# Kernel optimization log

Hardware: AMD Instinct MI355X
Metric: run time of the kernel (lower is better)

The kernel has to match this reference:

```python
import jax, jax.numpy as jnp
import numpy as np

N_NODES = 100000
HIDDEN = 64
N_LAYERS = 4
N_EDGES = 800000
EPS = 1e-5  # equinox RMSNorm default


def rmsnorm(x, w):
    # per-node RMSNorm over last dim, learned scale, no bias
    inv = jax.lax.rsqrt(jnp.mean(x * x, axis=-1, keepdims=True) + EPS)
    return x * inv * w


def setup_inputs() -> dict:
    key = jax.random.key(0)
    ks = jax.random.split(key, 5)
    x = jax.random.normal(ks[0], (N_NODES, HIDDEN), dtype=jnp.float32)
    # eqx Linear weight (out,in), init ~ U(-1/sqrt(in), 1/sqrt(in)); randn*scale is fine for a baseline
    scale = 1.0 / np.sqrt(HIDDEN)
    conv_w = jax.random.normal(ks[1], (N_LAYERS, HIDDEN, HIDDEN), dtype=jnp.float32) * scale
    hid_w = jax.random.normal(ks[2], (N_LAYERS, HIDDEN, HIDDEN), dtype=jnp.float32) * scale
    conv_norm_w = jnp.ones((N_LAYERS, HIDDEN), dtype=jnp.float32)
    hid_norm_w = jnp.ones((N_LAYERS, HIDDEN), dtype=jnp.float32)
    row = jax.random.randint(ks[3], (N_EDGES,), 0, N_NODES, dtype=jnp.int32)
    col = jax.random.randint(ks[4], (N_EDGES,), 0, N_NODES, dtype=jnp.int32)
    return {"x": x, "conv_w": conv_w, "conv_norm_w": conv_norm_w,
            "hid_w": hid_w, "hid_norm_w": hid_norm_w, "row": row, "col": col}


def reference(x, conv_w, conv_norm_w, hid_w, hid_norm_w, row, col):
    n_nodes = x.shape[0]

    def step(h, params):
        cw, cnw, hw, hnw = params
        # GConvLayer: linear (no bias) -> relu -> sparse adjacency aggregation -> residual RMSNorm
        m = jax.nn.relu(h @ cw.T)                                  # [n_nodes, d]
        agg = jax.ops.segment_sum(m[col], row, num_segments=n_nodes)  # a @ m (unweighted COO)
        h = rmsnorm(h + agg, cnw)
        # HiddenLayer: linear -> relu -> residual RMSNorm
        y = jax.nn.relu(h @ hw.T)
        h = rmsnorm(h + y, hnw)
        return h, None

    x, _ = jax.lax.scan(step, x, (conv_w, conv_norm_w, hid_w, hid_norm_w))
    return x
```

## Files before the change

kernel.cpp:

```cpp
#include <hip/hip_runtime.h>
#include <hip/hip_bf16.h>

#define HIDDEN 64
#define EPS 1e-5f
#define NPB 64
#define FNPB 32
#define WST 72

typedef __attribute__((ext_vector_type(8))) short bf16x8;
typedef __attribute__((ext_vector_type(4))) float f32x4;

__device__ __forceinline__ unsigned short f2b(float x) {
    __hip_bfloat16 b = __float2bfloat16(x);
    return *(unsigned short*)&b;
}
__device__ __forceinline__ float b2f(unsigned short u) {
    unsigned int ui = (unsigned int)u << 16;
    return *(float*)&ui;
}
__device__ __forceinline__ float b2f_lo(unsigned int u) { unsigned int ui = u << 16; return *(float*)&ui; }
__device__ __forceinline__ float b2f_hi(unsigned int u) { unsigned int ui = u & 0xffff0000u; return *(float*)&ui; }
__device__ __forceinline__ unsigned int pk2(float a, float b) {
    return (unsigned int)f2b(a) | ((unsigned int)f2b(b) << 16);
}


__global__ __launch_bounds__(256) void hist_rank_kernel(const int* __restrict__ row,
                                                        int* __restrict__ cnt,
                                                        int* __restrict__ erank, int e) {
    int stride = gridDim.x * blockDim.x;
    for (int i = blockIdx.x * blockDim.x + threadIdx.x; i < e; i += stride) {
        int r = row[i];
        erank[i] = atomicAdd(&cnt[r], 1);
    }
}

__global__ __launch_bounds__(256) void block_sum_kernel(const int* __restrict__ cnt,
                                                        int* __restrict__ bsum, int n) {
    __shared__ int wsum[4];
    int tid = threadIdx.x;
    int i = blockIdx.x * 256 + tid;
    int v = (i < n) ? cnt[i] : 0;
#pragma unroll
    for (int off = 32; off > 0; off >>= 1) v += __shfl_xor(v, off, 64);
    if ((tid & 63) == 0) wsum[tid >> 6] = v;
    __syncthreads();
    if (tid == 0) bsum[blockIdx.x] = wsum[0] + wsum[1] + wsum[2] + wsum[3];
}

__global__ __launch_bounds__(256) void scan_final_kernel(const int* __restrict__ cnt,
                                                         const int* __restrict__ bsum,
                                                         int* __restrict__ row_ptr,
                                                         int n, int nb) {
    __shared__ int wred[4];
    __shared__ int wsum[4];
    __shared__ int wexcl[4];
    __shared__ int s_prev;
    __shared__ int s_tot;
    int b = blockIdx.x;
    int tid = threadIdx.x;
    int lane = tid & 63;
    int w = tid >> 6;
    int acc = 0;
    for (int j = tid; j < b; j += 256) acc += bsum[j];
#pragma unroll
    for (int off = 32; off > 0; off >>= 1) acc += __shfl_xor(acc, off, 64);
    if (lane == 0) wred[w] = acc;
    int i = b * 256 + tid;
    int v = (i < n) ? cnt[i] : 0;
    int sc = v;
#pragma unroll
    for (int off = 1; off < 64; off <<= 1) {
        int t = __shfl_up(sc, off, 64);
        if (lane >= off) sc += t;
    }
    if (lane == 63) wsum[w] = sc;
    __syncthreads();
    if (tid == 0) {
        s_prev = wred[0] + wred[1] + wred[2] + wred[3];
        int a = 0;
#pragma unroll
        for (int j = 0; j < 4; j++) { wexcl[j] = a; a += wsum[j]; }
        s_tot = a;
    }
    __syncthreads();
    if (i < n) row_ptr[i] = s_prev + wexcl[w] + (sc - v);
    if (b == nb - 1 && tid == 0) row_ptr[n] = s_prev + s_tot;
}

__global__ __launch_bounds__(256) void fill_kernel(const int* __restrict__ row,
                                                   const int* __restrict__ col,
                                                   const int* __restrict__ row_ptr,
                                                   const int* __restrict__ erank,
                                                   int* __restrict__ ecol, int e, int n) {
    int cls = blockIdx.x & 7;
    int sub = blockIdx.x >> 3;
    int nsub = gridDim.x >> 3;
    int lo = (int)(((long long)n * cls) >> 3);
    int hi = (int)(((long long)n * (cls + 1)) >> 3);
    for (int i = sub * 256 + threadIdx.x; i < e; i += nsub * 256) {
        int r = row[i];
        if (r >= lo && r < hi) {
            int pos = row_ptr[r] + erank[i];
            ecol[pos] = col[i];
        }
    }
}

__global__ __launch_bounds__(256) void wconv_kernel(const float* __restrict__ cw,
                                                    const float* __restrict__ hw,
                                                    unsigned short* __restrict__ wbt,
                                                    unsigned short* __restrict__ mA,
                                                    unsigned short* __restrict__ mB,
                                                    int L, int n) {
    int idx = blockIdx.x * blockDim.x + threadIdx.x;
    int total = 2 * L * 4096;
    if (idx < total) {
        int mat = idx >> 12;
        int rem = idx & 4095;
        const float* src = (mat < L) ? (cw + (size_t)mat * 4096) : (hw + (size_t)(mat - L) * 4096);
        wbt[idx] = f2b(src[rem]);
    } else if (idx < total + HIDDEN) {
        int k = idx - total;
        mA[(size_t)n * HIDDEN + k] = 0;
        mB[(size_t)n * HIDDEN + k] = 0;
    }
}


__device__ __forceinline__ void mfma_tile(const unsigned short* s_a,
                                          const unsigned short* s_b,
                                          int l16, int quad, int wbase, f32x4 acc[4]) {
    const unsigned short* ap = &s_a[(size_t)(wbase + l16) * WST + quad * 8];
    const unsigned short* bp = &s_b[(size_t)l16 * WST + quad * 8];
#pragma unroll
    for (int kt = 0; kt < 2; kt++) {
        bf16x8 a = *(const bf16x8*)(ap + kt * 32);
#pragma unroll
        for (int nt = 0; nt < 4; nt++) {
            bf16x8 b = *(const bf16x8*)(bp + (size_t)nt * 16 * WST + kt * 32);
            acc[nt] = __builtin_amdgcn_mfma_f32_16x16x32_bf16(a, b, acc[nt], 0, 0, 0);
        }
    }
}

__device__ __forceinline__ void load_wfrag(const unsigned short* __restrict__ w,
                                           int l16, int quad, bf16x8 wf[8]) {
    const unsigned short* wp = w + (size_t)l16 * 64 + quad * 8;
#pragma unroll
    for (int nt = 0; nt < 4; nt++) {
#pragma unroll
        for (int kt = 0; kt < 2; kt++)
            wf[nt * 2 + kt] = *(const bf16x8*)(wp + (size_t)nt * 16 * 64 + kt * 32);
    }
}

__device__ __forceinline__ void stage_wb(const unsigned short* __restrict__ wsrc,
                                         unsigned short* s_wb, int tid) {
    for (int i = tid; i < 512; i += 256) {
        int r = i >> 3, seg = i & 7;
        *(uint4*)(&s_wb[r * WST + seg * 8]) = ((const uint4*)(wsrc + r * 64))[seg];
    }
}

__device__ __forceinline__ void acc8(float* p, uint4 u) {
    p[0] += b2f_lo(u.x);
    p[1] += b2f_hi(u.x);
    p[2] += b2f_lo(u.y);
    p[3] += b2f_hi(u.y);
    p[4] += b2f_lo(u.z);
    p[5] += b2f_hi(u.z);
    p[6] += b2f_lo(u.w);
    p[7] += b2f_hi(u.w);
}


__global__ __launch_bounds__(256) void mm_relu_kernel(const float* __restrict__ h,
                                                      const unsigned short* __restrict__ wb,
                                                      __hip_bfloat16* __restrict__ m, int n) {
    __shared__ unsigned short s_hb[NPB * WST];
    __shared__ unsigned short s_wb[64 * WST];
    int tid = threadIdx.x;
    int base = blockIdx.x * NPB;
    stage_wb(wb, s_wb, tid);
    for (int i = tid; i < 512; i += 256) {
        int r = i >> 3, seg = i & 7;
        if (base + r < n) {
            const float4* hp = (const float4*)(h + (size_t)(base + r) * HIDDEN + seg * 8);
            float4 ha = hp[0], hb = hp[1];
            uint4 p;
            p.x = pk2(ha.x, ha.y);
            p.y = pk2(ha.z, ha.w);
            p.z = pk2(hb.x, hb.y);
            p.w = pk2(hb.z, hb.w);
            *(uint4*)(&s_hb[r * WST + seg * 8]) = p;
        } else {
            *(uint4*)(&s_hb[r * WST + seg * 8]) = make_uint4(0u, 0u, 0u, 0u);
        }
    }
    __syncthreads();
    int lane = tid & 63, wave = tid >> 6;
    int quad = lane >> 4, l16 = lane & 15;
    int wbase = wave * 16;
    f32x4 acc[4];
    acc[0] = (f32x4){0.f,0.f,0.f,0.f}; acc[1] = (f32x4){0.f,0.f,0.f,0.f};
    acc[2] = (f32x4){0.f,0.f,0.f,0.f}; acc[3] = (f32x4){0.f,0.f,0.f,0.f};
    mfma_tile(s_hb, s_wb, l16, quad, wbase, acc);
    unsigned short* mo = (unsigned short*)m;
#pragma unroll
    for (int r = 0; r < 4; r++) {
        int node = base + wbase + quad * 4 + r;
        if (node < n) {
#pragma unroll
            for (int nt = 0; nt < 4; nt++)
                mo[(size_t)node * HIDDEN + nt * 16 + l16] = f2b(fmaxf(acc[nt][r], 0.f));
        }
    }
}


__global__ __launch_bounds__(128, 6) void fused_layer_kernel(
        const float* hf, const __hip_bfloat16* hb_in,
        const __hip_bfloat16* __restrict__ m_in,
        const unsigned short* __restrict__ hwb,
        const unsigned short* cwb_next,
        const int* __restrict__ row_ptr, const int* __restrict__ ecol,
        const float* __restrict__ cnw, const float* __restrict__ hnw,
        float* out_f32, __hip_bfloat16* hb_new, __hip_bfloat16* m_out, int n) {
    __shared__ unsigned short s_hb[FNPB * WST];
    int tid = threadIdx.x;
    int base = blockIdx.x * FNPB;
    int lane = tid & 63, wave = tid >> 6;

    int g = lane >> 2;
    int sl = lane & 3;
    int gb = lane & ~3;
    int nl = wave * 16 + g;
    int node = base + nl;

    const unsigned short* mi = (const unsigned short*)m_in;

    uint4 q0 = make_uint4(0u, 0u, 0u, 0u);
    uint4 q1 = make_uint4(0u, 0u, 0u, 0u);
    if (node < n) {
        float p[16];
        if (hf) {
            const float4* hp = (const float4*)(hf + (size_t)node * HIDDEN + 16 * sl);
            float4 v0 = hp[0], v1 = hp[1], v2 = hp[2], v3 = hp[3];
            p[0]=v0.x;  p[1]=v0.y;  p[2]=v0.z;  p[3]=v0.w;
            p[4]=v1.x;  p[5]=v1.y;  p[6]=v1.z;  p[7]=v1.w;
            p[8]=v2.x;  p[9]=v2.y;  p[10]=v2.z; p[11]=v2.w;
            p[12]=v3.x; p[13]=v3.y; p[14]=v3.z; p[15]=v3.w;
        } else {
            const uint4* hp = (const uint4*)((const unsigned short*)hb_in + (size_t)node * HIDDEN + 16 * sl);
            uint4 u0 = hp[0], u1 = hp[1];
            p[0]=b2f_lo(u0.x);  p[1]=b2f_hi(u0.x);
            p[2]=b2f_lo(u0.y);  p[3]=b2f_hi(u0.y);
            p[4]=b2f_lo(u0.z);  p[5]=b2f_hi(u0.z);
            p[6]=b2f_lo(u0.w);  p[7]=b2f_hi(u0.w);
            p[8]=b2f_lo(u1.x);  p[9]=b2f_hi(u1.x);
            p[10]=b2f_lo(u1.y); p[11]=b2f_hi(u1.y);
            p[12]=b2f_lo(u1.z); p[13]=b2f_hi(u1.z);
            p[14]=b2f_lo(u1.w); p[15]=b2f_hi(u1.w);
        }
        int beg = row_ptr[node];
        int end = row_ptr[node + 1];
        int myc = 0;
        if (beg < end) {
            int idx = beg + sl;
            myc = ecol[idx < end ? idx : end - 1];
        }
        for (int b0 = beg; b0 < end; b0 += 4) {
            int nxt = b0 + 4;
            int nmyc = 0;
            if (nxt < end) {
                int idx = nxt + sl;
                nmyc = ecol[idx < end ? idx : end - 1];
            }
            int cnt = end - b0;
            int cj[4];
#pragma unroll
            for (int j = 0; j < 4; j++) {
                int c = __shfl(myc, gb + j, 64);
                cj[j] = (j < cnt) ? c : n;
            }
            uint4 ua[4], ub[4];
#pragma unroll
            for (int j = 0; j < 4; j++) {
                const uint4* mp = (const uint4*)(mi + (size_t)cj[j] * HIDDEN + 16 * sl);
                ua[j] = mp[0];
                ub[j] = mp[1];
            }
#pragma unroll
            for (int j = 0; j < 4; j++) {
                acc8(p, ua[j]);
                acc8(p + 8, ub[j]);
            }
            myc = nmyc;
        }
        float ss = 0.f;
#pragma unroll
        for (int k = 0; k < 16; k++) ss += p[k] * p[k];
        ss += __shfl_xor(ss, 1, 64);
        ss += __shfl_xor(ss, 2, 64);
        float inv = rsqrtf(ss * (1.0f / 64.0f) + EPS);
        const float4* cp = (const float4*)(cnw + 16 * sl);
        float4 c0 = cp[0], c1 = cp[1], c2 = cp[2], c3 = cp[3];
        q0.x = pk2(p[0]*inv*c0.x,  p[1]*inv*c0.y);
        q0.y = pk2(p[2]*inv*c0.z,  p[3]*inv*c0.w);
        q0.z = pk2(p[4]*inv*c1.x,  p[5]*inv*c1.y);
        q0.w = pk2(p[6]*inv*c1.z,  p[7]*inv*c1.w);
        q1.x = pk2(p[8]*inv*c2.x,  p[9]*inv*c2.y);
        q1.y = pk2(p[10]*inv*c2.z, p[11]*inv*c2.w);
        q1.z = pk2(p[12]*inv*c3.x, p[13]*inv*c3.y);
        q1.w = pk2(p[14]*inv*c3.z, p[15]*inv*c3.w);
    }
    *(uint4*)(&s_hb[(size_t)nl * WST + 16 * sl]) = q0;
    *(uint4*)(&s_hb[(size_t)nl * WST + 16 * sl + 8]) = q1;

    int quad = lane >> 4, l16 = lane & 15;
    int wbase = wave * 16;
    bf16x8 wfh[8];
    load_wfrag(hwb, l16, quad, wfh);
    f32x4 acc[4];
    acc[0] = (f32x4){0.f,0.f,0.f,0.f}; acc[1] = (f32x4){0.f,0.f,0.f,0.f};
    acc[2] = (f32x4){0.f,0.f,0.f,0.f}; acc[3] = (f32x4){0.f,0.f,0.f,0.f};
    {
        const unsigned short* ap = &s_hb[(size_t)(wbase + l16) * WST + quad * 8];
#pragma unroll
        for (int kt = 0; kt < 2; kt++) {
            bf16x8 a = *(const bf16x8*)(ap + kt * 32);
#pragma unroll
            for (int nt = 0; nt < 4; nt++)
                acc[nt] = __builtin_amdgcn_mfma_f32_16x16x32_bf16(a, wfh[nt * 2 + kt], acc[nt], 0, 0, 0);
        }
    }

    float hv[4][4];
    float ssq[4] = {0.f, 0.f, 0.f, 0.f};
#pragma unroll
    for (int r = 0; r < 4; r++) {
        int nr = wbase + quad * 4 + r;
#pragma unroll
        for (int nt = 0; nt < 4; nt++) {
            float hres = b2f(s_hb[(size_t)nr * WST + nt * 16 + l16]);
            float v = hres + fmaxf(acc[nt][r], 0.f);
            hv[r][nt] = v;
            ssq[r] += v * v;
        }
    }
#pragma unroll
    for (int mk = 1; mk <= 8; mk <<= 1) {
#pragma unroll
        for (int r = 0; r < 4; r++) ssq[r] += __shfl_xor(ssq[r], mk, 64);
    }
    bf16x8 wfc[8];
    if (m_out) load_wfrag(cwb_next, l16, quad, wfc);
    float nwv[4];
#pragma unroll
    for (int nt = 0; nt < 4; nt++) nwv[nt] = hnw[nt * 16 + l16];
#pragma unroll
    for (int r = 0; r < 4; r++) {
        float inv = rsqrtf(ssq[r] * (1.0f / 64.0f) + EPS);
#pragma unroll
        for (int nt = 0; nt < 4; nt++) hv[r][nt] *= inv * nwv[nt];
    }
    if (out_f32) {
#pragma unroll
        for (int r = 0; r < 4; r++) {
            int nd = base + wbase + quad * 4 + r;
            if (nd < n) {
#pragma unroll
                for (int nt = 0; nt < 4; nt++)
                    out_f32[(size_t)nd * HIDDEN + nt * 16 + l16] = hv[r][nt];
            }
        }
    }
    if (hb_new) {
        unsigned short* ho = (unsigned short*)hb_new;
#pragma unroll
        for (int r = 0; r < 4; r++) {
            int nd = base + wbase + quad * 4 + r;
            if (nd < n) {
#pragma unroll
                for (int nt = 0; nt < 4; nt++)
                    ho[(size_t)nd * HIDDEN + nt * 16 + l16] = f2b(hv[r][nt]);
            }
        }
    }

    if (!m_out) return;

#pragma unroll
    for (int r = 0; r < 4; r++) {
        int nr = wbase + quad * 4 + r;
#pragma unroll
        for (int nt = 0; nt < 4; nt++)
            s_hb[(size_t)nr * WST + nt * 16 + l16] = f2b(hv[r][nt]);
    }

    f32x4 acc2[4];
    acc2[0] = (f32x4){0.f,0.f,0.f,0.f}; acc2[1] = (f32x4){0.f,0.f,0.f,0.f};
    acc2[2] = (f32x4){0.f,0.f,0.f,0.f}; acc2[3] = (f32x4){0.f,0.f,0.f,0.f};
    {
        const unsigned short* ap = &s_hb[(size_t)(wbase + l16) * WST + quad * 8];
#pragma unroll
        for (int kt = 0; kt < 2; kt++) {
            bf16x8 a = *(const bf16x8*)(ap + kt * 32);
#pragma unroll
            for (int nt = 0; nt < 4; nt++)
                acc2[nt] = __builtin_amdgcn_mfma_f32_16x16x32_bf16(a, wfc[nt * 2 + kt], acc2[nt], 0, 0, 0);
        }
    }
    unsigned short* mo = (unsigned short*)m_out;
#pragma unroll
    for (int r = 0; r < 4; r++) {
        int nd = base + wbase + quad * 4 + r;
        if (nd < n) {
#pragma unroll
            for (int nt = 0; nt < 4; nt++)
                mo[(size_t)nd * HIDDEN + nt * 16 + l16] = f2b(fmaxf(acc2[nt][r], 0.f));
        }
    }
}


static inline size_t align_up(size_t x, size_t a) { return (x + a - 1) & ~(a - 1); }

extern "C" void kernel_launch(void* const* d_in, const int* in_sizes, int n_in,
                              void* d_out, int out_size, void* d_ws, size_t ws_size,
                              hipStream_t stream) {
    const float* x       = (const float*)d_in[0];
    const float* conv_w  = (const float*)d_in[1];
    const float* conv_nw = (const float*)d_in[2];
    const float* hid_w   = (const float*)d_in[3];
    const float* hid_nw  = (const float*)d_in[4];
    const int*   row     = (const int*)d_in[5];
    const int*   col     = (const int*)d_in[6];
    float* out = (float*)d_out;

    const int n = in_sizes[0] / HIDDEN;
    const int e = in_sizes[5];
    const int L = in_sizes[1] / 4096;

    size_t off = 0;
    char* ws = (char*)d_ws;
    __hip_bfloat16* mA = (__hip_bfloat16*)(ws + off);  off = align_up(off + (size_t)(n + 1) * HIDDEN * 2, 16);
    __hip_bfloat16* mB = (__hip_bfloat16*)(ws + off);  off = align_up(off + (size_t)(n + 1) * HIDDEN * 2, 16);
    __hip_bfloat16* hb1 = (__hip_bfloat16*)(ws + off); off = align_up(off + (size_t)n * HIDDEN * 2, 16);
    __hip_bfloat16* hb2 = (__hip_bfloat16*)(ws + off); off = align_up(off + (size_t)n * HIDDEN * 2, 16);
    unsigned short* wbt = (unsigned short*)(ws + off); off = align_up(off + (size_t)2 * L * 4096 * 2, 16);
    int* row_ptr = (int*)(ws + off);           off = align_up(off + (size_t)(n + 1) * 4, 16);
    int* cnt = (int*)(ws + off);               off = align_up(off + (size_t)n * 4, 16);
    int* bsum = (int*)(ws + off);              off = align_up(off + (size_t)1024 * 4, 16);
    int* erank = (int*)(ws + off);             off = align_up(off + (size_t)e * 4, 16);
    int* ecol = (int*)(ws + off);              off = align_up(off + (size_t)e * 4, 16);

    const int nb = (n + 255) / 256;

    hipMemsetAsync(cnt, 0, (size_t)n * 4, stream);
    hist_rank_kernel<<<1024, 256, 0, stream>>>(row, cnt, erank, e);
    block_sum_kernel<<<nb, 256, 0, stream>>>(cnt, bsum, n);
    scan_final_kernel<<<nb, 256, 0, stream>>>(cnt, bsum, row_ptr, n, nb);
    fill_kernel<<<1024, 256, 0, stream>>>(row, col, row_ptr, erank, ecol, e, n);

    wconv_kernel<<<(2 * L * 4096 + HIDDEN + 255) / 256, 256, 0, stream>>>(
        conv_w, hid_w, wbt, (unsigned short*)mA, (unsigned short*)mB, L, n);

    mm_relu_kernel<<<(n + NPB - 1) / NPB, 256, 0, stream>>>(x, wbt, mA, n);

    const int fblocks = (n + FNPB - 1) / FNPB;
    const __hip_bfloat16* mi = mA;
    __hip_bfloat16* mo = mB;
    __hip_bfloat16* hin = nullptr;
    __hip_bfloat16* hout = hb1;
    for (int l = 0; l < L; l++) {
        bool last = (l == L - 1);
        fused_layer_kernel<<<fblocks, 128, 0, stream>>>(
            (l == 0) ? x : nullptr, hin, mi,
            wbt + (size_t)(L + l) * 4096,
            last ? nullptr : (wbt + (size_t)(l + 1) * 4096),
            row_ptr, ecol,
            conv_nw + (size_t)l * HIDDEN, hid_nw + (size_t)l * HIDDEN,
            last ? out : nullptr,
            last ? nullptr : hout,
            last ? nullptr : mo, n);
        __hip_bfloat16* tmp = (__hip_bfloat16*)mi; mi = mo; mo = tmp;
        hin = hout;
        hout = (hout == hb1) ? hb2 : hb1;
    }
}
```

Baseline: 296.6 us.

## Merge CSR build into cooperative kernel and use 8 lanes per node in gather

Folds the memset, histogram, two scan passes, fill and weight conversion into one cooperative kernel separated by grid syncs, which cuts launch count. The fused layer kernel now uses 256 threads with 8 lanes per node, each handling 8 features and 8 edges per step. This gives more memory-level parallelism in the gather but half-fills each MFMA tile with padded zero rows. The fill pass also drops the row-range partitioning, so its writes become scattered.

New measurement: 798.3 us. 169% more time.

```diff
diff --git a/kernel.cpp b/kernel.cpp
--- a/kernel.cpp
+++ b/kernel.cpp
@@ -1,5 +1,8 @@
 #include <hip/hip_runtime.h>
 #include <hip/hip_bf16.h>
+#include <hip/hip_cooperative_groups.h>
+
+namespace cg = cooperative_groups;
 
 #define HIDDEN 64
 #define EPS 1e-5f
@@ -25,105 +28,88 @@
 }
 
 
-__global__ __launch_bounds__(256) void hist_rank_kernel(const int* __restrict__ row,
-                                                        int* __restrict__ cnt,
-                                                        int* __restrict__ erank, int e) {
-    int stride = gridDim.x * blockDim.x;
-    for (int i = blockIdx.x * blockDim.x + threadIdx.x; i < e; i += stride) {
-        int r = row[i];
-        erank[i] = atomicAdd(&cnt[r], 1);
-    }
-}
-
-__global__ __launch_bounds__(256) void block_sum_kernel(const int* __restrict__ cnt,
-                                                        int* __restrict__ bsum, int n) {
+__global__ __launch_bounds__(256) void csr_coop_kernel(
+        const int* __restrict__ row, const int* __restrict__ col,
+        const float* __restrict__ cw, const float* __restrict__ hw,
+        int* cnt, int* erank, int* bsum, int* row_ptr, int* ecol,
+        unsigned short* wbt, unsigned short* mA, unsigned short* mB,
+        int n, int e, int L, int nb) {
+    cg::grid_group grid = cg::this_grid();
     __shared__ int wsum[4];
-    int tid = threadIdx.x;
-    int i = blockIdx.x * 256 + tid;
-    int v = (i < n) ? cnt[i] : 0;
-#pragma unroll
-    for (int off = 32; off > 0; off >>= 1) v += __shfl_xor(v, off, 64);
-    if ((tid & 63) == 0) wsum[tid >> 6] = v;
-    __syncthreads();
-    if (tid == 0) bsum[blockIdx.x] = wsum[0] + wsum[1] + wsum[2] + wsum[3];
-}
-
-__global__ __launch_bounds__(256) void scan_final_kernel(const int* __restrict__ cnt,
-                                                         const int* __restrict__ bsum,
-                                                         int* __restrict__ row_ptr,
-                                                         int n, int nb) {
     __shared__ int wred[4];
-    __shared__ int wsum[4];
     __shared__ int wexcl[4];
     __shared__ int s_prev;
     __shared__ int s_tot;
-    int b = blockIdx.x;
     int tid = threadIdx.x;
-    int lane = tid & 63;
-    int w = tid >> 6;
-    int acc = 0;
-    for (int j = tid; j < b; j += 256) acc += bsum[j];
-#pragma unroll
-    for (int off = 32; off > 0; off >>= 1) acc += __shfl_xor(acc, off, 64);
-    if (lane == 0) wred[w] = acc;
-    int i = b * 256 + tid;
-    int v = (i < n) ? cnt[i] : 0;
-    int sc = v;
-#pragma unroll
-    for (int off = 1; off < 64; off <<= 1) {
-        int t = __shfl_up(sc, off, 64);
-        if (lane >= off) sc += t;
-    }
-    if (lane == 63) wsum[w] = sc;
-    __syncthreads();
-    if (tid == 0) {
-        s_prev = wred[0] + wred[1] + wred[2] + wred[3];
-        int a = 0;
-#pragma unroll
-        for (int j = 0; j < 4; j++) { wexcl[j] = a; a += wsum[j]; }
-        s_tot = a;
-    }
-    __syncthreads();
-    if (i < n) row_ptr[i] = s_prev + wexcl[w] + (sc - v);
-    if (b == nb - 1 && tid == 0) row_ptr[n] = s_prev + s_tot;
-}
-
-__global__ __launch_bounds__(256) void fill_kernel(const int* __restrict__ row,
-                                                   const int* __restrict__ col,
-                                                   const int* __restrict__ row_ptr,
-                                                   const int* __restrict__ erank,
-                                                   int* __restrict__ ecol, int e, int n) {
-    int cls = blockIdx.x & 7;
-    int sub = blockIdx.x >> 3;
-    int nsub = gridDim.x >> 3;
-    int lo = (int)(((long long)n * cls) >> 3);
-    int hi = (int)(((long long)n * (cls + 1)) >> 3);
-    for (int i = sub * 256 + threadIdx.x; i < e; i += nsub * 256) {
+    int gid = blockIdx.x * 256 + tid;
+    int gstride = gridDim.x * 256;
+
+    for (int i = gid; i < n; i += gstride) cnt[i] = 0;
+    int total = 2 * L * 4096;
+    for (int i = gid; i < total; i += gstride) {
+        int mat = i >> 12;
+        int rem = i & 4095;
+        const float* src = (mat < L) ? (cw + (size_t)mat * 4096) : (hw + (size_t)(mat - L) * 4096);
+        wbt[i] = f2b(src[rem]);
+    }
+    if (gid < HIDDEN) {
+        mA[(size_t)n * HIDDEN + gid] = 0;
+        mB[(size_t)n * HIDDEN + gid] = 0;
+    }
+    grid.sync();
+
+    for (int i = gid; i < e; i += gstride) {
         int r = row[i];
-        if (r >= lo && r < hi) {
-            int pos = row_ptr[r] + erank[i];
-            ecol[pos] = col[i];
-        }
-    }
-}
-
-__global__ __launch_bounds__(256) void wconv_kernel(const float* __restrict__ cw,
-                                                    const float* __restrict__ hw,
-                                                    unsigned short* __restrict__ wbt,
-                                                    unsigned short* __restrict__ mA,
-                                                    unsigned short* __restrict__ mB,
-                                                    int L, int n) {
-    int idx = blockIdx.x * blockDim.x + threadIdx.x;
-    int total = 2 * L * 4096;
-    if (idx < total) {
-        int mat = idx >> 12;
-        int rem = idx & 4095;
-        const float* src = (mat < L) ? (cw + (size_t)mat * 4096) : (hw + (size_t)(mat - L) * 4096);
-        wbt[idx] = f2b(src[rem]);
-    } else if (idx < total + HIDDEN) {
-        int k = idx - total;
-        mA[(size_t)n * HIDDEN + k] = 0;
-        mB[(size_t)n * HIDDEN + k] = 0;
+        erank[i] = atomicAdd(&cnt[r], 1);
+    }
+    grid.sync();
+
+    for (int c = blockIdx.x; c < nb; c += gridDim.x) {
+        int i = c * 256 + tid;
+        int v = (i < n) ? cnt[i] : 0;
+#pragma unroll
+        for (int off = 32; off > 0; off >>= 1) v += __shfl_xor(v, off, 64);
+        if ((tid & 63) == 0) wsum[tid >> 6] = v;
+        __syncthreads();
+        if (tid == 0) bsum[c] = wsum[0] + wsum[1] + wsum[2] + wsum[3];
+        __syncthreads();
+    }
+    grid.sync();
+
+    for (int c = blockIdx.x; c < nb; c += gridDim.x) {
+        int lane = tid & 63, w = tid >> 6;
+        int acc = 0;
+        for (int j = tid; j < c; j += 256) acc += bsum[j];
+#pragma unroll
+        for (int off = 32; off > 0; off >>= 1) acc += __shfl_xor(acc, off, 64);
+        if (lane == 0) wred[w] = acc;
+        int i = c * 256 + tid;
+        int v = (i < n) ? cnt[i] : 0;
+        int sc = v;
+#pragma unroll
+        for (int off = 1; off < 64; off <<= 1) {
+            int t = __shfl_up(sc, off, 64);
+            if (lane >= off) sc += t;
+        }
+        if (lane == 63) wsum[w] = sc;
+        __syncthreads();
+        if (tid == 0) {
+            s_prev = wred[0] + wred[1] + wred[2] + wred[3];
+            int a = 0;
+#pragma unroll
+            for (int j = 0; j < 4; j++) { wexcl[j] = a; a += wsum[j]; }
+            s_tot = a;
+        }
+        __syncthreads();
+        if (i < n) row_ptr[i] = s_prev + wexcl[w] + (sc - v);
+        if (c == nb - 1 && tid == 0) row_ptr[n] = s_prev + s_tot;
+        __syncthreads();
+    }
+    grid.sync();
+
+    for (int i = gid; i < e; i += gstride) {
+        int r = row[i];
+        ecol[row_ptr[r] + erank[i]] = col[i];
     }
 }
 
@@ -219,7 +205,7 @@
 }
 
 
-__global__ __launch_bounds__(128, 6) void fused_layer_kernel(
+__global__ __launch_bounds__(256, 6) void fused_layer_kernel(
         const float* hf, const __hip_bfloat16* hb_in,
         const __hip_bfloat16* __restrict__ m_in,
         const unsigned short* __restrict__ hwb,
@@ -227,41 +213,35 @@
         const int* __restrict__ row_ptr, const int* __restrict__ ecol,
         const float* __restrict__ cnw, const float* __restrict__ hnw,
         float* out_f32, __hip_bfloat16* hb_new, __hip_bfloat16* m_out, int n) {
-    __shared__ unsigned short s_hb[FNPB * WST];
+    __shared__ unsigned short s_hb[64 * WST];
     int tid = threadIdx.x;
     int base = blockIdx.x * FNPB;
     int lane = tid & 63, wave = tid >> 6;
 
-    int g = lane >> 2;
-    int sl = lane & 3;
-    int gb = lane & ~3;
+    int g = lane >> 3;
+    int sl = lane & 7;
+    int gb = lane & ~7;
     int nl = wave * 16 + g;
-    int node = base + nl;
+    int node = base + wave * 8 + g;
+
+    *(uint4*)(&s_hb[(size_t)(wave * 16 + 8 + g) * WST + 8 * sl]) = make_uint4(0u, 0u, 0u, 0u);
 
     const unsigned short* mi = (const unsigned short*)m_in;
 
     uint4 q0 = make_uint4(0u, 0u, 0u, 0u);
-    uint4 q1 = make_uint4(0u, 0u, 0u, 0u);
     if (node < n) {
-        float p[16];
+        float p[8];
         if (hf) {
-            const float4* hp = (const float4*)(hf + (size_t)node * HIDDEN + 16 * sl);
-            float4 v0 = hp[0], v1 = hp[1], v2 = hp[2], v3 = hp[3];
-            p[0]=v0.x;  p[1]=v0.y;  p[2]=v0.z;  p[3]=v0.w;
-            p[4]=v1.x;  p[5]=v1.y;  p[6]=v1.z;  p[7]=v1.w;
-            p[8]=v2.x;  p[9]=v2.y;  p[10]=v2.z; p[11]=v2.w;
-            p[12]=v3.x; p[13]=v3.y; p[14]=v3.z; p[15]=v3.w;
+            const float4* hp = (const float4*)(hf + (size_t)node * HIDDEN + 8 * sl);
+            float4 v0 = hp[0], v1 = hp[1];
+            p[0]=v0.x; p[1]=v0.y; p[2]=v0.z; p[3]=v0.w;
+            p[4]=v1.x; p[5]=v1.y; p[6]=v1.z; p[7]=v1.w;
         } else {
-            const uint4* hp = (const uint4*)((const unsigned short*)hb_in + (size_t)node * HIDDEN + 16 * sl);
-            uint4 u0 = hp[0], u1 = hp[1];
-            p[0]=b2f_lo(u0.x);  p[1]=b2f_hi(u0.x);
-            p[2]=b2f_lo(u0.y);  p[3]=b2f_hi(u0.y);
-            p[4]=b2f_lo(u0.z);  p[5]=b2f_hi(u0.z);
-            p[6]=b2f_lo(u0.w);  p[7]=b2f_hi(u0.w);
-            p[8]=b2f_lo(u1.x);  p[9]=b2f_hi(u1.x);
-            p[10]=b2f_lo(u1.y); p[11]=b2f_hi(u1.y);
-            p[12]=b2f_lo(u1.z); p[13]=b2f_hi(u1.z);
-            p[14]=b2f_lo(u1.w); p[15]=b2f_hi(u1.w);
+            uint4 u0 = *(const uint4*)((const unsigned short*)hb_in + (size_t)node * HIDDEN + 8 * sl);
+            p[0]=b2f_lo(u0.x); p[1]=b2f_hi(u0.x);
+            p[2]=b2f_lo(u0.y); p[3]=b2f_hi(u0.y);
+            p[4]=b2f_lo(u0.z); p[5]=b2f_hi(u0.z);
+            p[6]=b2f_lo(u0.w); p[7]=b2f_hi(u0.w);
         }
         int beg = row_ptr[node];
         int end = row_ptr[node + 1];
@@ -270,53 +250,44 @@
             int idx = beg + sl;
             myc = ecol[idx < end ? idx : end - 1];
         }
-        for (int b0 = beg; b0 < end; b0 += 4) {
-            int nxt = b0 + 4;
+        for (int b0 = beg; b0 < end; b0 += 8) {
+            int nxt = b0 + 8;
             int nmyc = 0;
             if (nxt < end) {
                 int idx = nxt + sl;
                 nmyc = ecol[idx < end ? idx : end - 1];
             }
             int cnt = end - b0;
-            int cj[4];
-#pragma unroll
-            for (int j = 0; j < 4; j++) {
+            int cj[8];
+#pragma unroll
+            for (int j = 0; j < 8; j++) {
                 int c = __shfl(myc, gb + j, 64);
                 cj[j] = (j < cnt) ? c : n;
             }
-            uint4 ua[4], ub[4];
-#pragma unroll
-            for (int j = 0; j < 4; j++) {
-                const uint4* mp = (const uint4*)(mi + (size_t)cj[j] * HIDDEN + 16 * sl);
-                ua[j] = mp[0];
-                ub[j] = mp[1];
-            }
-#pragma unroll
-            for (int j = 0; j < 4; j++) {
-                acc8(p, ua[j]);
-                acc8(p + 8, ub[j]);
-            }
+            uint4 u[8];
+#pragma unroll
+            for (int j = 0; j < 8; j++)
+                u[j] = *(const uint4*)(mi + (size_t)cj[j] * HIDDEN + 8 * sl);
+#pragma unroll
+            for (int j = 0; j < 8; j++)
+                acc8(p, u[j]);
             myc = nmyc;
         }
         float ss = 0.f;
 #pragma unroll
-        for (int k = 0; k < 16; k++) ss += p[k] * p[k];
+        for (int k = 0; k < 8; k++) ss += p[k] * p[k];
         ss += __shfl_xor(ss, 1, 64);
         ss += __shfl_xor(ss, 2, 64);
+        ss += __shfl_xor(ss, 4, 64);
         float inv = rsqrtf(ss * (1.0f / 64.0f) + EPS);
-        const float4* cp = (const float4*)(cnw + 16 * sl);
-        float4 c0 = cp[0], c1 = cp[1], c2 = cp[2], c3 = cp[3];
-        q0.x = pk2(p[0]*inv*c0.x,  p[1]*inv*c0.y);
-        q0.y = pk2(p[2]*inv*c0.z,  p[3]*inv*c0.w);
-        q0.z = pk2(p[4]*inv*c1.x,  p[5]*inv*c1.y);
-        q0.w = pk2(p[6]*inv*c1.z,  p[7]*inv*c1.w);
-        q1.x = pk2(p[8]*inv*c2.x,  p[9]*inv*c2.y);
-        q1.y = pk2(p[10]*inv*c2.z, p[11]*inv*c2.w);
-        q1.z = pk2(p[12]*inv*c3.x, p[13]*inv*c3.y);
-        q1.w = pk2(p[14]*inv*c3.z, p[15]*inv*c3.w);
-    }
-    *(uint4*)(&s_hb[(size_t)nl * WST + 16 * sl]) = q0;
-    *(uint4*)(&s_hb[(size_t)nl * WST + 16 * sl + 8]) = q1;
+        const float4* cp = (const float4*)(cnw + 8 * sl);
+        float4 c0 = cp[0], c1 = cp[1];
+        q0.x = pk2(p[0]*inv*c0.x, p[1]*inv*c0.y);
+        q0.y = pk2(p[2]*inv*c0.z, p[3]*inv*c0.w);
+        q0.z = pk2(p[4]*inv*c1.x, p[5]*inv*c1.y);
+        q0.w = pk2(p[6]*inv*c1.z, p[7]*inv*c1.w);
+    }
+    *(uint4*)(&s_hb[(size_t)nl * WST + 8 * sl]) = q0;
 
     int quad = lane >> 4, l16 = lane & 15;
     int wbase = wave * 16;
@@ -368,8 +339,9 @@
     if (out_f32) {
 #pragma unroll
         for (int r = 0; r < 4; r++) {
-            int nd = base + wbase + quad * 4 + r;
-            if (nd < n) {
+            int rr = quad * 4 + r;
+            int nd = base + wave * 8 + rr;
+            if (rr < 8 && nd < n) {
 #pragma unroll
                 for (int nt = 0; nt < 4; nt++)
                     out_f32[(size_t)nd * HIDDEN + nt * 16 + l16] = hv[r][nt];
@@ -380,8 +352,9 @@
         unsigned short* ho = (unsigned short*)hb_new;
 #pragma unroll
         for (int r = 0; r < 4; r++) {
-            int nd = base + wbase + quad * 4 + r;
-            if (nd < n) {
+            int rr = quad * 4 + r;
+            int nd = base + wave * 8 + rr;
+            if (rr < 8 && nd < n) {
 #pragma unroll
                 for (int nt = 0; nt < 4; nt++)
                     ho[(size_t)nd * HIDDEN + nt * 16 + l16] = f2b(hv[r][nt]);
@@ -415,8 +388,9 @@
     unsigned short* mo = (unsigned short*)m_out;
 #pragma unroll
     for (int r = 0; r < 4; r++) {
-        int nd = base + wbase + quad * 4 + r;
-        if (nd < n) {
+        int rr = quad * 4 + r;
+        int nd = base + wave * 8 + rr;
+        if (rr < 8 && nd < n) {
 #pragma unroll
             for (int nt = 0; nt < 4; nt++)
                 mo[(size_t)nd * HIDDEN + nt * 16 + l16] = f2b(fmaxf(acc2[nt][r], 0.f));
@@ -458,14 +432,28 @@
 
     const int nb = (n + 255) / 256;
 
-    hipMemsetAsync(cnt, 0, (size_t)n * 4, stream);
-    hist_rank_kernel<<<1024, 256, 0, stream>>>(row, cnt, erank, e);
-    block_sum_kernel<<<nb, 256, 0, stream>>>(cnt, bsum, n);
-    scan_final_kernel<<<nb, 256, 0, stream>>>(cnt, bsum, row_ptr, n, nb);
-    fill_kernel<<<1024, 256, 0, stream>>>(row, col, row_ptr, erank, ecol, e, n);
-
-    wconv_kernel<<<(2 * L * 4096 + HIDDEN + 255) / 256, 256, 0, stream>>>(
-        conv_w, hid_w, wbt, (unsigned short*)mA, (unsigned short*)mB, L, n);
+    {
+        const int* row_a = row;
+        const int* col_a = col;
+        const float* cw_a = conv_w;
+        const float* hw_a = hid_w;
+        int* cnt_a = cnt;
+        int* erank_a = erank;
+        int* bsum_a = bsum;
+        int* rp_a = row_ptr;
+        int* ecol_a = ecol;
+        unsigned short* wbt_a = wbt;
+        unsigned short* mA_a = (unsigned short*)mA;
+        unsigned short* mB_a = (unsigned short*)mB;
+        int n_a = n, e_a = e, L_a = L, nb_a = nb;
+        void* cargs[] = {
+            (void*)&row_a, (void*)&col_a, (void*)&cw_a, (void*)&hw_a,
+            (void*)&cnt_a, (void*)&erank_a, (void*)&bsum_a, (void*)&rp_a, (void*)&ecol_a,
+            (void*)&wbt_a, (void*)&mA_a, (void*)&mB_a,
+            (void*)&n_a, (void*)&e_a, (void*)&L_a, (void*)&nb_a };
+        hipLaunchCooperativeKernel((const void*)csr_coop_kernel,
+                                   dim3(1024), dim3(256), cargs, 0, stream);
+    }
 
     mm_relu_kernel<<<(n + NPB - 1) / NPB, 256, 0, stream>>>(x, wbt, mA, n);
 
@@ -476,7 +464,7 @@
     __hip_bfloat16* hout = hb1;
     for (int l = 0; l < L; l++) {
         bool last = (l == L - 1);
-        fused_layer_kernel<<<fblocks, 128, 0, stream>>>(
+        fused_layer_kernel<<<fblocks, 256, 0, stream>>>(
             (l == 0) ? x : nullptr, hin, mi,
             wbt + (size_t)(L + l) * 4096,
             last ? nullptr : (wbt + (size_t)(l + 1) * 4096),
```

## Merge setup kernels, shrink fused layer blocks, and double-buffer neighbor gathers

Applied to the files above, without the earlier changes.

Merges the histogram pass with weight conversion, and the CSR fill with the first matmul+ReLU, into single launches using block-index ranges, which removes two kernel launches and lets independent work overlap. The fused layer kernel now uses one 64-thread wave per block covering 16 nodes, in place of two waves covering 32. The neighbor gather loop is software-pipelined so the next group of four rows is loaded while the current one is accumulated. The trade-offs are higher register pressure from the in-flight buffers, more blocks to schedule, and MFMA weight fragments reloaded across twice as many blocks.

Measured after the change: 330.5 us. 11.4% more time.

```diff
diff --git a/kernel.cpp b/kernel.cpp
--- a/kernel.cpp
+++ b/kernel.cpp
@@ -4,7 +4,7 @@
 #define HIDDEN 64
 #define EPS 1e-5f
 #define NPB 64
-#define FNPB 32
+#define FNPB 16
 #define WST 72
 
 typedef __attribute__((ext_vector_type(8))) short bf16x8;
@@ -25,13 +25,32 @@
 }
 
 
-__global__ __launch_bounds__(256) void hist_rank_kernel(const int* __restrict__ row,
-                                                        int* __restrict__ cnt,
-                                                        int* __restrict__ erank, int e) {
-    int stride = gridDim.x * blockDim.x;
-    for (int i = blockIdx.x * blockDim.x + threadIdx.x; i < e; i += stride) {
-        int r = row[i];
-        erank[i] = atomicAdd(&cnt[r], 1);
+__global__ __launch_bounds__(256) void hist_wconv_kernel(
+        const int* __restrict__ row, int* __restrict__ cnt, int* __restrict__ erank, int e,
+        const float* __restrict__ cw, const float* __restrict__ hw,
+        unsigned short* __restrict__ wbt,
+        unsigned short* __restrict__ mA, unsigned short* __restrict__ mB,
+        int L, int n) {
+    int b = blockIdx.x;
+    if (b < 1024) {
+        int stride = 1024 * 256;
+        for (int i = b * 256 + threadIdx.x; i < e; i += stride) {
+            int r = row[i];
+            erank[i] = atomicAdd(&cnt[r], 1);
+        }
+    } else {
+        int idx = (b - 1024) * 256 + threadIdx.x;
+        int total = 2 * L * 4096;
+        if (idx < total) {
+            int mat = idx >> 12;
+            int rem = idx & 4095;
+            const float* src = (mat < L) ? (cw + (size_t)mat * 4096) : (hw + (size_t)(mat - L) * 4096);
+            wbt[idx] = f2b(src[rem]);
+        } else if (idx < total + HIDDEN) {
+            int k = idx - total;
+            mA[(size_t)n * HIDDEN + k] = 0;
+            mB[(size_t)n * HIDDEN + k] = 0;
+        }
     }
 }
 
@@ -88,45 +107,6 @@
     if (b == nb - 1 && tid == 0) row_ptr[n] = s_prev + s_tot;
 }
 
-__global__ __launch_bounds__(256) void fill_kernel(const int* __restrict__ row,
-                                                   const int* __restrict__ col,
-                                                   const int* __restrict__ row_ptr,
-                                                   const int* __restrict__ erank,
-                                                   int* __restrict__ ecol, int e, int n) {
-    int cls = blockIdx.x & 7;
-    int sub = blockIdx.x >> 3;
-    int nsub = gridDim.x >> 3;
-    int lo = (int)(((long long)n * cls) >> 3);
-    int hi = (int)(((long long)n * (cls + 1)) >> 3);
-    for (int i = sub * 256 + threadIdx.x; i < e; i += nsub * 256) {
-        int r = row[i];
-        if (r >= lo && r < hi) {
-            int pos = row_ptr[r] + erank[i];
-            ecol[pos] = col[i];
-        }
-    }
-}
-
-__global__ __launch_bounds__(256) void wconv_kernel(const float* __restrict__ cw,
-                                                    const float* __restrict__ hw,
-                                                    unsigned short* __restrict__ wbt,
-                                                    unsigned short* __restrict__ mA,
-                                                    unsigned short* __restrict__ mB,
-                                                    int L, int n) {
-    int idx = blockIdx.x * blockDim.x + threadIdx.x;
-    int total = 2 * L * 4096;
-    if (idx < total) {
-        int mat = idx >> 12;
-        int rem = idx & 4095;
-        const float* src = (mat < L) ? (cw + (size_t)mat * 4096) : (hw + (size_t)(mat - L) * 4096);
-        wbt[idx] = f2b(src[rem]);
-    } else if (idx < total + HIDDEN) {
-        int k = idx - total;
-        mA[(size_t)n * HIDDEN + k] = 0;
-        mB[(size_t)n * HIDDEN + k] = 0;
-    }
-}
-
 
 __device__ __forceinline__ void mfma_tile(const unsigned short* s_a,
                                           const unsigned short* s_b,
@@ -174,13 +154,45 @@
     p[7] += b2f_hi(u.w);
 }
 
-
-__global__ __launch_bounds__(256) void mm_relu_kernel(const float* __restrict__ h,
-                                                      const unsigned short* __restrict__ wb,
-                                                      __hip_bfloat16* __restrict__ m, int n) {
+__device__ __forceinline__ void gather4(const unsigned short* __restrict__ mi,
+                                        int ec, int cnt, int gb, int sl, int n,
+                                        uint4 ua[4], uint4 ub[4]) {
+#pragma unroll
+    for (int j = 0; j < 4; j++) {
+        int c = __shfl(ec, gb + j, 64);
+        int cj = (j < cnt) ? c : n;
+        const uint4* mp = (const uint4*)(mi + (size_t)cj * HIDDEN + 16 * sl);
+        ua[j] = mp[0];
+        ub[j] = mp[1];
+    }
+}
+
+
+__global__ __launch_bounds__(256) void fill_mm_kernel(
+        const int* __restrict__ row, const int* __restrict__ col,
+        const int* __restrict__ row_ptr, const int* __restrict__ erank,
+        int* __restrict__ ecol, int e, int n,
+        const float* __restrict__ h, const unsigned short* __restrict__ wb,
+        __hip_bfloat16* __restrict__ m, int mmblocks) {
     __shared__ unsigned short s_hb[NPB * WST];
     __shared__ unsigned short s_wb[64 * WST];
     int tid = threadIdx.x;
+    if ((int)blockIdx.x >= mmblocks) {
+        int bid = blockIdx.x - mmblocks;
+        int cls = bid & 7;
+        int sub = bid >> 3;
+        int nsub = 128;
+        int lo = (int)(((long long)n * cls) >> 3);
+        int hi = (int)(((long long)n * (cls + 1)) >> 3);
+        for (int i = sub * 256 + tid; i < e; i += nsub * 256) {
+            int r = row[i];
+            if (r >= lo && r < hi) {
+                int pos = row_ptr[r] + erank[i];
+                ecol[pos] = col[i];
+            }
+        }
+        return;
+    }
     int base = blockIdx.x * NPB;
     stage_wb(wb, s_wb, tid);
     for (int i = tid; i < 512; i += 256) {
@@ -219,7 +231,7 @@
 }
 
 
-__global__ __launch_bounds__(128, 6) void fused_layer_kernel(
+__global__ __launch_bounds__(64, 5) void fused_layer_kernel(
         const float* hf, const __hip_bfloat16* hb_in,
         const __hip_bfloat16* __restrict__ m_in,
         const unsigned short* __restrict__ hwb,
@@ -228,15 +240,13 @@
         const float* __restrict__ cnw, const float* __restrict__ hnw,
         float* out_f32, __hip_bfloat16* hb_new, __hip_bfloat16* m_out, int n) {
     __shared__ unsigned short s_hb[FNPB * WST];
-    int tid = threadIdx.x;
+    int lane = threadIdx.x & 63;
     int base = blockIdx.x * FNPB;
-    int lane = tid & 63, wave = tid >> 6;
 
     int g = lane >> 2;
     int sl = lane & 3;
     int gb = lane & ~3;
-    int nl = wave * 16 + g;
-    int node = base + nl;
+    int node = base + g;
 
     const unsigned short* mi = (const unsigned short*)m_in;
 
@@ -265,38 +275,36 @@
         }
         int beg = row_ptr[node];
         int end = row_ptr[node + 1];
-        int myc = 0;
         if (beg < end) {
-            int idx = beg + sl;
-            myc = ecol[idx < end ? idx : end - 1];
-        }
-        for (int b0 = beg; b0 < end; b0 += 4) {
-            int nxt = b0 + 4;
-            int nmyc = 0;
-            if (nxt < end) {
-                int idx = nxt + sl;
-                nmyc = ecol[idx < end ? idx : end - 1];
-            }
-            int cnt = end - b0;
-            int cj[4];
-#pragma unroll
-            for (int j = 0; j < 4; j++) {
-                int c = __shfl(myc, gb + j, 64);
-                cj[j] = (j < cnt) ? c : n;
+            int idx0 = beg + sl;
+            int ec_cur = ecol[idx0 < end ? idx0 : end - 1];
+            int ec_nxt = 0;
+            if (beg + 4 < end) {
+                int idx1 = beg + 4 + sl;
+                ec_nxt = ecol[idx1 < end ? idx1 : end - 1];
             }
             uint4 ua[4], ub[4];
-#pragma unroll
-            for (int j = 0; j < 4; j++) {
-                const uint4* mp = (const uint4*)(mi + (size_t)cj[j] * HIDDEN + 16 * sl);
-                ua[j] = mp[0];
-                ub[j] = mp[1];
+            gather4(mi, ec_cur, end - beg, gb, sl, n, ua, ub);
+            for (int b0 = beg; b0 < end; b0 += 4) {
+                int n1 = b0 + 4;
+                int n2 = b0 + 8;
+                int ec_nn = 0;
+                if (n2 < end) {
+                    int idx = n2 + sl;
+                    ec_nn = ecol[idx < end ? idx : end - 1];
+                }
+                bool have_next = (n1 < end);
+                uint4 na[4], nb[4];
+                if (have_next)
+                    gather4(mi, ec_nxt, end - n1, gb, sl, n, na, nb);
+#pragma unroll
+                for (int j = 0; j < 4; j++) { acc8(p, ua[j]); acc8(p + 8, ub[j]); }
+                if (have_next) {
+#pragma unroll
+                    for (int j = 0; j < 4; j++) { ua[j] = na[j]; ub[j] = nb[j]; }
+                }
+                ec_nxt = ec_nn;
             }
-#pragma unroll
-            for (int j = 0; j < 4; j++) {
-                acc8(p, ua[j]);
-                acc8(p + 8, ub[j]);
-            }
-            myc = nmyc;
         }
         float ss = 0.f;
 #pragma unroll
@@ -315,18 +323,17 @@
         q1.z = pk2(p[12]*inv*c3.x, p[13]*inv*c3.y);
         q1.w = pk2(p[14]*inv*c3.z, p[15]*inv*c3.w);
     }
-    *(uint4*)(&s_hb[(size_t)nl * WST + 16 * sl]) = q0;
-    *(uint4*)(&s_hb[(size_t)nl * WST + 16 * sl + 8]) = q1;
+    *(uint4*)(&s_hb[(size_t)g * WST + 16 * sl]) = q0;
+    *(uint4*)(&s_hb[(size_t)g * WST + 16 * sl + 8]) = q1;
 
     int quad = lane >> 4, l16 = lane & 15;
-    int wbase = wave * 16;
     bf16x8 wfh[8];
     load_wfrag(hwb, l16, quad, wfh);
     f32x4 acc[4];
     acc[0] = (f32x4){0.f,0.f,0.f,0.f}; acc[1] = (f32x4){0.f,0.f,0.f,0.f};
     acc[2] = (f32x4){0.f,0.f,0.f,0.f}; acc[3] = (f32x4){0.f,0.f,0.f,0.f};
     {
-        const unsigned short* ap = &s_hb[(size_t)(wbase + l16) * WST + quad * 8];
+        const unsigned short* ap = &s_hb[(size_t)l16 * WST + quad * 8];
 #pragma unroll
         for (int kt = 0; kt < 2; kt++) {
             bf16x8 a = *(const bf16x8*)(ap + kt * 32);
@@ -340,7 +347,7 @@
     float ssq[4] = {0.f, 0.f, 0.f, 0.f};
 #pragma unroll
     for (int r = 0; r < 4; r++) {
-        int nr = wbase + quad * 4 + r;
+        int nr = quad * 4 + r;
 #pragma unroll
         for (int nt = 0; nt < 4; nt++) {
             float hres = b2f(s_hb[(size_t)nr * WST + nt * 16 + l16]);
@@ -368,7 +375,7 @@
     if (out_f32) {
 #pragma unroll
         for (int r = 0; r < 4; r++) {
-            int nd = base + wbase + quad * 4 + r;
+            int nd = base + quad * 4 + r;
             if (nd < n) {
 #pragma unroll
                 for (int nt = 0; nt < 4; nt++)
@@ -380,7 +387,7 @@
         unsigned short* ho = (unsigned short*)hb_new;
 #pragma unroll
         for (int r = 0; r < 4; r++) {
-            int nd = base + wbase + quad * 4 + r;
+            int nd = base + quad * 4 + r;
             if (nd < n) {
 #pragma unroll
                 for (int nt = 0; nt < 4; nt++)
@@ -393,7 +400,7 @@
 
 #pragma unroll
     for (int r = 0; r < 4; r++) {
-        int nr = wbase + quad * 4 + r;
+        int nr = quad * 4 + r;
 #pragma unroll
         for (int nt = 0; nt < 4; nt++)
             s_hb[(size_t)nr * WST + nt * 16 + l16] = f2b(hv[r][nt]);
@@ -403,7 +410,7 @@
     acc2[0] = (f32x4){0.f,0.f,0.f,0.f}; acc2[1] = (f32x4){0.f,0.f,0.f,0.f};
     acc2[2] = (f32x4){0.f,0.f,0.f,0.f}; acc2[3] = (f32x4){0.f,0.f,0.f,0.f};
     {
-        const unsigned short* ap = &s_hb[(size_t)(wbase + l16) * WST + quad * 8];
+        const unsigned short* ap = &s_hb[(size_t)l16 * WST + quad * 8];
 #pragma unroll
         for (int kt = 0; kt < 2; kt++) {
             bf16x8 a = *(const bf16x8*)(ap + kt * 32);
@@ -415,7 +422,7 @@
     unsigned short* mo = (unsigned short*)m_out;
 #pragma unroll
     for (int r = 0; r < 4; r++) {
-        int nd = base + wbase + quad * 4 + r;
+        int nd = base + quad * 4 + r;
         if (nd < n) {
 #pragma unroll
             for (int nt = 0; nt < 4; nt++)
@@ -457,17 +464,17 @@
     int* ecol = (int*)(ws + off);              off = align_up(off + (size_t)e * 4, 16);
 
     const int nb = (n + 255) / 256;
+    const int wconv_blocks = (2 * L * 4096 + HIDDEN + 255) / 256;
+    const int mmblocks = (n + NPB - 1) / NPB;
 
     hipMemsetAsync(cnt, 0, (size_t)n * 4, stream);
-    hist_rank_kernel<<<1024, 256, 0, stream>>>(row, cnt, erank, e);
+    hist_wconv_kernel<<<1024 + wconv_blocks, 256, 0, stream>>>(
+        row, cnt, erank, e, conv_w, hid_w, wbt,
+        (unsigned short*)mA, (unsigned short*)mB, L, n);
     block_sum_kernel<<<nb, 256, 0, stream>>>(cnt, bsum, n);
     scan_final_kernel<<<nb, 256, 0, stream>>>(cnt, bsum, row_ptr, n, nb);
-    fill_kernel<<<1024, 256, 0, stream>>>(row, col, row_ptr, erank, ecol, e, n);
-
-    wconv_kernel<<<(2 * L * 4096 + HIDDEN + 255) / 256, 256, 0, stream>>>(
-        conv_w, hid_w, wbt, (unsigned short*)mA, (unsigned short*)mB, L, n);
-
-    mm_relu_kernel<<<(n + NPB - 1) / NPB, 256, 0, stream>>>(x, wbt, mA, n);
+    fill_mm_kernel<<<mmblocks + 1024, 256, 0, stream>>>(
+        row, col, row_ptr, erank, ecol, e, n, x, wbt, mA, mmblocks);
 
     const int fblocks = (n + FNPB - 1) / FNPB;
     const __hip_bfloat16* mi = mA;
@@ -476,7 +483,7 @@
     __hip_bfloat16* hout = hb1;
     for (int l = 0; l < L; l++) {
         bool last = (l == L - 1);
-        fused_layer_kernel<<<fblocks, 128, 0, stream>>>(
+        fused_layer_kernel<<<fblocks, 64, 0, stream>>>(
             (l == 0) ? x : nullptr, hin, mi,
             wbt + (size_t)(L + l) * 4096,
             last ? nullptr : (wbt + (size_t)(l + 1) * 4096),
```
